# Kernel tuning notes

Measured on AMD Instinct MI355X. Metric: run time of the kernel, lower is better.

The kernel has to match this reference:

```python
import jax, jax.numpy as jnp
import numpy as np

B, DIM, HEADS, BLOCKS = 16, 192, 6, 6
H = W = 64
WS, SHIFT, MLP = 8, 4, 4
N = WS * WS
HD = DIM // HEADS
NW = (H // WS) * (W // WS)
SCALE = HD ** -0.5


def _ln(x, g, b, eps=1e-5):
    mu = jnp.mean(x, -1, keepdims=True)
    var = jnp.mean(jnp.square(x - mu), -1, keepdims=True)
    return (x - mu) * jax.lax.rsqrt(var + eps) * g + b


def _win_part(x):  # [B,H,W,C] -> [B*NW, N, C]
    x = x.reshape(B, H // WS, WS, W // WS, WS, DIM)
    return x.transpose(0, 1, 3, 2, 4, 5).reshape(-1, N, DIM)


def _win_rev(w):  # [B*NW, N, C] -> [B,H,W,C]
    x = w.reshape(B, H // WS, W // WS, WS, WS, DIM)
    return x.transpose(0, 1, 3, 2, 4, 5).reshape(B, H, W, DIM)


def _rel_pos_index():
    coords = np.stack(np.meshgrid(np.arange(WS), np.arange(WS), indexing='ij')).reshape(2, -1)
    rel = (coords[:, :, None] - coords[:, None, :]).transpose(1, 2, 0)
    rel[:, :, 0] += WS - 1
    rel[:, :, 1] += WS - 1
    rel[:, :, 0] *= 2 * WS - 1
    return jnp.asarray(rel.sum(-1))  # [N, N] int


def _attn_mask():  # shifted-window attention mask, [NW, N, N]
    img = np.zeros((H, W))
    cnt = 0
    for hs in (slice(0, -WS), slice(-WS, -SHIFT), slice(-SHIFT, None)):
        for ws_ in (slice(0, -WS), slice(-WS, -SHIFT), slice(-SHIFT, None)):
            img[hs, ws_] = cnt
            cnt += 1
    mw = img.reshape(H // WS, WS, W // WS, WS).transpose(0, 2, 1, 3).reshape(-1, N)
    am = mw[:, None, :] - mw[:, :, None]
    return jnp.asarray(np.where(am != 0, -100.0, 0.0).astype(np.float32))


RPI = _rel_pos_index()
MASK = _attn_mask()


def _block(x, shifted, n1g, n1b, qkvw, qkvb, pw, pb, rpb, n2g, n2b, f1w, f1b, f2w, f2b):
    shortcut = x  # [B, H*W, DIM]
    x = _ln(x, n1g, n1b).reshape(B, H, W, DIM)
    if shifted:
        x = jnp.roll(x, (-SHIFT, -SHIFT), (1, 2))
    xw = _win_part(x)  # [B*NW, N, DIM]
    qkv = (xw @ qkvw.T + qkvb).reshape(-1, N, 3, HEADS, HD).transpose(2, 0, 3, 1, 4)
    q, k, v = qkv[0], qkv[1], qkv[2]  # [B*NW, HEADS, N, HD]
    attn = jnp.einsum('bhnd,bhmd->bhnm', q * SCALE, k)
    attn = attn + rpb[RPI].transpose(2, 0, 1)[None]  # relative position bias
    if shifted:
        attn = (attn.reshape(B, NW, HEADS, N, N) + MASK[None, :, None]).reshape(-1, HEADS, N, N)
    attn = jax.nn.softmax(attn, -1)
    xw = jnp.einsum('bhnm,bhmd->bnhd', attn, v).reshape(-1, N, DIM)
    xw = xw @ pw.T + pb
    x = _win_rev(xw)
    if shifted:
        x = jnp.roll(x, (SHIFT, SHIFT), (1, 2))
    x = shortcut + x.reshape(B, H * W, DIM)
    h = _ln(x, n2g, n2b)
    h = jax.nn.gelu(h @ f1w.T + f1b, approximate=False) @ f2w.T + f2b
    return x + h


def _forward(x, en_g, en_b, n1_g, n1_b, qkv_w, qkv_b, proj_w, proj_b, rpb, n2_g, n2_b, fc1_w, fc1_b, fc2_w, fc2_b, fn_g, fn_b, conv_w):
    y = x.reshape(B, DIM, H * W).transpose(0, 2, 1)  # patch embed (patch_size=1)
    y = _ln(y, en_g, en_b)
    for i in range(BLOCKS):
        y = _block(y, i % 2 == 1, n1_g[i], n1_b[i], qkv_w[i], qkv_b[i], proj_w[i], proj_b[i],
                   rpb[i], n2_g[i], n2_b[i], fc1_w[i], fc1_b[i], fc2_w[i], fc2_b[i])
    y = _ln(y, fn_g, fn_b)
    y = y.transpose(0, 2, 1).reshape(B, DIM, H, W)  # patch unembed
    return y + jax.lax.conv_general_dilated(y, conv_w, (1, 1), 'SAME',
                                            dimension_numbers=('NCHW', 'OIHW', 'NCHW'))


def setup_inputs() -> dict:
    key = jax.random.key(0)
    ks = jax.random.split(key, 7)
    s = 0.02
    f32 = jnp.float32
    return {
        'x': jax.random.normal(ks[0], (B, DIM, H, W), f32),
        'en_g': jnp.ones((DIM,), f32), 'en_b': jnp.zeros((DIM,), f32),
        'n1_g': jnp.ones((BLOCKS, DIM), f32), 'n1_b': jnp.zeros((BLOCKS, DIM), f32),
        'qkv_w': s * jax.random.normal(ks[1], (BLOCKS, 3 * DIM, DIM), f32),
        'qkv_b': jnp.zeros((BLOCKS, 3 * DIM), f32),
        'proj_w': s * jax.random.normal(ks[2], (BLOCKS, DIM, DIM), f32),
        'proj_b': jnp.zeros((BLOCKS, DIM), f32),
        'rpb': s * jax.random.normal(ks[3], (BLOCKS, (2 * WS - 1) ** 2, HEADS), f32),
        'n2_g': jnp.ones((BLOCKS, DIM), f32), 'n2_b': jnp.zeros((BLOCKS, DIM), f32),
        'fc1_w': s * jax.random.normal(ks[4], (BLOCKS, MLP * DIM, DIM), f32),
        'fc1_b': jnp.zeros((BLOCKS, MLP * DIM), f32),
        'fc2_w': s * jax.random.normal(ks[5], (BLOCKS, DIM, MLP * DIM), f32),
        'fc2_b': jnp.zeros((BLOCKS, DIM), f32),
        'fn_g': jnp.ones((DIM,), f32), 'fn_b': jnp.zeros((DIM,), f32),
        'conv_w': s * jax.random.normal(ks[6], (DIM, DIM, 3, 3), f32),
    }


def reference(x, en_g, en_b, n1_g, n1_b, qkv_w, qkv_b, proj_w, proj_b, rpb, n2_g, n2_b, fc1_w, fc1_b, fc2_w, fc2_b, fn_g, fn_b, conv_w):
    return _forward(x, en_g, en_b, n1_g, n1_b, qkv_w, qkv_b, proj_w, proj_b, rpb,
                    n2_g, n2_b, fc1_w, fc1_b, fc2_w, fc2_b, fn_g, fn_b, conv_w)
```

## Files before the change

kernel.cpp:

```cpp
#include <hip/hip_runtime.h>
#include <cstdint>
#include <cstddef>

#define BATCH 16
#define DIM 192
#define HEADS 6
#define HD 32
#define TOK 65536
#define QKV_D 576
#define MLP_D 768
#define SCALE 0.17677669529663687f

#define CHQ 32768

typedef __bf16 bf16x8 __attribute__((ext_vector_type(8)));
typedef float f32x4 __attribute__((ext_vector_type(4)));

__device__ __forceinline__ unsigned short f2bf(float f) {
  union { float f; unsigned u; } c;
  c.f = f;
  return (unsigned short)((c.u + 0x7fffu + ((c.u >> 16) & 1)) >> 16);
}

__device__ __forceinline__ float waveSum(float v) {
#pragma unroll
  for (int off = 32; off; off >>= 1) v += __shfl_xor(v, off, 64);
  return v;
}

__device__ __forceinline__ float rowSum16(float v) {
  v += __shfl_xor(v, 1, 64);
  v += __shfl_xor(v, 2, 64);
  v += __shfl_xor(v, 4, 64);
  v += __shfl_xor(v, 8, 64);
  return v;
}

#define GLD(SRC, DST)                                                     \
  __builtin_amdgcn_global_load_lds(                                       \
      (const __attribute__((address_space(1))) void*)(SRC),               \
      (__attribute__((address_space(3))) void*)(DST), 16, 0, 0)

__global__ __launch_bounds__(64) void zero_k(float* p) { p[threadIdx.x] = 0.f; }

__global__ __launch_bounds__(256) void cvt_k(const float* __restrict__ s,
                                             unsigned short* __restrict__ d,
                                             int n) {
  int i = ((blockIdx.x << 8) + threadIdx.x) << 2;
  if (i < n) {
    float4 v = *(const float4*)(s + i);
    d[i] = f2bf(v.x);
    d[i + 1] = f2bf(v.y);
    d[i + 2] = f2bf(v.z);
    d[i + 3] = f2bf(v.w);
  }
}

__global__ __launch_bounds__(256) void cvt_qkv_k(const float* __restrict__ s,
                                                 unsigned short* __restrict__ d) {
  int i = (blockIdx.x << 8) + threadIdx.x;
  if (i < 663552) {
    int r = (i / 192) % 576;
    float v = s[i];
    if (r < 192) v *= SCALE;
    d[i] = f2bf(v);
  }
}

__global__ __launch_bounds__(256) void scale_qkvb_k(const float* __restrict__ s,
                                                    float* __restrict__ d) {
  int i = (blockIdx.x << 8) + threadIdx.x;
  if (i < 3456) {
    float v = s[i];
    if ((i % 576) < 192) v *= SCALE;
    d[i] = v;
  }
}

__global__ __launch_bounds__(256) void cvt_conv_k(const float* __restrict__ s,
                                                  unsigned short* __restrict__ d) {
  int i = (blockIdx.x << 8) + threadIdx.x;
  if (i < 331776) {
    int o = i / 1728;
    int r = i - o * 1728;
    int tap = r / 192;
    int ci = r - tap * 192;
    d[i] = f2bf(s[o * 1728 + ci * 9 + tap]);
  }
}

__global__ __launch_bounds__(256) void embed_ln_t_k(
    const float* __restrict__ x, const float* __restrict__ g,
    const float* __restrict__ be, float* __restrict__ y) {
  __shared__ float ts[192 * 65];
  const int w = threadIdx.x >> 6, lane = threadIdx.x & 63;
  const int t0 = blockIdx.x << 6;
  const int b = t0 >> 12, tb = t0 & 4095;
  const float* xb = x + (((size_t)b * DIM) << 12) + tb;
#pragma unroll
  for (int j = 0; j < 48; ++j) {
    int ch = w * 48 + j;
    ts[ch * 65 + lane] = xb[((size_t)ch << 12) + lane];
  }
  __syncthreads();
#pragma unroll 4
  for (int idx = 0; idx < 16; ++idx) {
    int tk = (w << 4) + idx;
    float v0 = ts[lane * 65 + tk];
    float v1 = ts[(lane + 64) * 65 + tk];
    float v2 = ts[(lane + 128) * 65 + tk];
    float mu = waveSum(v0 + v1 + v2) * (1.f / 192.f);
    float d0 = v0 - mu, d1 = v1 - mu, d2 = v2 - mu;
    float var = waveSum(d0 * d0 + d1 * d1 + d2 * d2) * (1.f / 192.f);
    float rs = rsqrtf(var + 1e-5f);
    float* yp = y + (size_t)(t0 + tk) * DIM;
    yp[lane] = d0 * rs * g[lane] + be[lane];
    yp[lane + 64] = d1 * rs * g[lane + 64] + be[lane + 64];
    yp[lane + 128] = d2 * rs * g[lane + 128] + be[lane + 128];
  }
}

__global__ __launch_bounds__(256) void ln_window_k(
    const float* __restrict__ y, const float* __restrict__ g,
    const float* __restrict__ be, unsigned short* __restrict__ xw,
    int shifted) {
  int m = (blockIdx.x << 2) + (threadIdx.x >> 6);
  int lane = threadIdx.x & 63;
  int widx = m >> 6, n = m & 63;
  int b = widx >> 6, win = widx & 63;
  int hp = ((win >> 3) << 3) + (n >> 3);
  int wp = ((win & 7) << 3) + (n & 7);
  if (shifted) { hp = (hp + 4) & 63; wp = (wp + 4) & 63; }
  int src = (b << 12) + (hp << 6) + wp;
  const float* yp = y + (size_t)src * DIM;
  float v0 = yp[lane], v1 = yp[lane + 64], v2 = yp[lane + 128];
  float mu = waveSum(v0 + v1 + v2) * (1.f / 192.f);
  float d0 = v0 - mu, d1 = v1 - mu, d2 = v2 - mu;
  float var = waveSum(d0 * d0 + d1 * d1 + d2 * d2) * (1.f / 192.f);
  float rs = rsqrtf(var + 1e-5f);
  unsigned short* op = xw + (size_t)m * DIM;
  op[lane] = f2bf(d0 * rs * g[lane] + be[lane]);
  op[lane + 64] = f2bf(d1 * rs * g[lane + 64] + be[lane + 64]);
  op[lane + 128] = f2bf(d2 * rs * g[lane + 128] + be[lane + 128]);
}

__global__ __launch_bounds__(64) void attn_k(
    const unsigned short* __restrict__ qkv, const float* __restrict__ rpb,
    unsigned short* __restrict__ out, int shifted, int widx0) {
  __shared__ unsigned short vt[32 * 72];
  __shared__ unsigned short pl[64 * 72];
  __shared__ float rp[228];
  const int lwidx = blockIdx.x / HEADS;
  const int head = blockIdx.x - lwidx * HEADS;
  const int l = threadIdx.x;
  const int g = l >> 4, li = l & 15;

  for (int i = l; i < 225; i += 64) rp[i] = rpb[i * HEADS + head];

  const unsigned short* base = qkv + (size_t)lwidx * 64 * QKV_D + head * HD;

  bf16x8 qf[4], kf[4];
#pragma unroll
  for (int n = 0; n < 4; ++n)
    qf[n] = *(const bf16x8*)(base + (size_t)(16 * n + li) * QKV_D + g * 8);
#pragma unroll
  for (int i = 0; i < 4; ++i)
    kf[i] = *(const bf16x8*)(base + (size_t)(16 * i + li) * QKV_D + DIM + g * 8);

#pragma unroll
  for (int p = 0; p < 4; ++p) {
    int r = 16 * p + (l >> 2);
    int d0 = (l & 3) << 3;
    bf16x8 v8 = *(const bf16x8*)(base + (size_t)r * QKV_D + 2 * DIM + d0);
#pragma unroll
    for (int e = 0; e < 8; ++e)
      vt[(d0 + e) * 72 + r] = ((const unsigned short*)&v8)[e];
  }

  f32x4 s[4][4] = {};
#pragma unroll
  for (int i = 0; i < 4; ++i)
#pragma unroll
    for (int n = 0; n < 4; ++n)
      s[i][n] = __builtin_amdgcn_mfma_f32_16x16x32_bf16(kf[i], qf[n], s[i][n],
                                                        0, 0, 0);
  __syncthreads();

  const int win = (widx0 + lwidx) & 63;
  const int wh = (win >> 3) << 3, wwp = (win & 7) << 3;
  int rq[4], cq[4], zq[4];
#pragma unroll
  for (int n = 0; n < 4; ++n) {
    int q = 16 * n + li;
    rq[n] = q >> 3;
    cq[n] = q & 7;
    zq[n] = 0;
    if (shifted) {
      int hq = wh + rq[n], wq = wwp + cq[n];
      int zr = hq < 56 ? 0 : (hq < 60 ? 1 : 2);
      int zc = wq < 56 ? 0 : (wq < 60 ? 1 : 2);
      zq[n] = 3 * zr + zc;
    }
  }
#pragma unroll
  for (int i = 0; i < 4; ++i)
#pragma unroll
    for (int j = 0; j < 4; ++j) {
      int m = 16 * i + 4 * g + j;
      int rm = m >> 3, cm = m & 7;
      int zm = 0;
      if (shifted) {
        int hm = wh + rm, wm = wwp + cm;
        int zr = hm < 56 ? 0 : (hm < 60 ? 1 : 2);
        int zc = wm < 56 ? 0 : (wm < 60 ? 1 : 2);
        zm = 3 * zr + zc;
      }
#pragma unroll
      for (int n = 0; n < 4; ++n) {
        float b = rp[(rq[n] - rm + 7) * 15 + (cq[n] - cm + 7)];
        if (shifted && zm != zq[n]) b -= 100.f;
        s[i][n][j] += b;
      }
    }

  float inv[4];
#pragma unroll
  for (int n = 0; n < 4; ++n) {
    float m0 = -1e30f;
#pragma unroll
    for (int i = 0; i < 4; ++i)
#pragma unroll
      for (int j = 0; j < 4; ++j) m0 = fmaxf(m0, s[i][n][j]);
    m0 = fmaxf(m0, __shfl_xor(m0, 16, 64));
    m0 = fmaxf(m0, __shfl_xor(m0, 32, 64));
    float s0 = 0.f;
#pragma unroll
    for (int i = 0; i < 4; ++i)
#pragma unroll
      for (int j = 0; j < 4; ++j) {
        float e = __expf(s[i][n][j] - m0);
        s[i][n][j] = e;
        s0 += e;
      }
    s0 += __shfl_xor(s0, 16, 64);
    s0 += __shfl_xor(s0, 32, 64);
    inv[n] = 1.f / s0;
  }

#pragma unroll
  for (int n = 0; n < 4; ++n) {
    int q = 16 * n + li;
#pragma unroll
    for (int i = 0; i < 4; ++i) {
      unsigned lo = (unsigned)f2bf(s[i][n][0]) | ((unsigned)f2bf(s[i][n][1]) << 16);
      unsigned hi = (unsigned)f2bf(s[i][n][2]) | ((unsigned)f2bf(s[i][n][3]) << 16);
      *(uint2*)&pl[q * 72 + 16 * i + 4 * g] = uint2{lo, hi};
    }
  }
  __syncthreads();

  f32x4 o[2][4] = {};
#pragma unroll
  for (int ks = 0; ks < 2; ++ks) {
    bf16x8 va[2], pb[4];
#pragma unroll
    for (int i2 = 0; i2 < 2; ++i2)
      va[i2] = *(const bf16x8*)&vt[(16 * i2 + li) * 72 + 32 * ks + 8 * g];
#pragma unroll
    for (int n2 = 0; n2 < 4; ++n2)
      pb[n2] = *(const bf16x8*)&pl[(16 * n2 + li) * 72 + 32 * ks + 8 * g];
#pragma unroll
    for (int i2 = 0; i2 < 2; ++i2)
#pragma unroll
      for (int n2 = 0; n2 < 4; ++n2)
        o[i2][n2] = __builtin_amdgcn_mfma_f32_16x16x32_bf16(va[i2], pb[n2],
                                                            o[i2][n2], 0, 0, 0);
  }

  unsigned short* ob = out + (size_t)(lwidx * 64) * DIM + head * HD;
#pragma unroll
  for (int i2 = 0; i2 < 2; ++i2)
#pragma unroll
    for (int n2 = 0; n2 < 4; ++n2) {
      int q = 16 * n2 + li;
      float iv = inv[n2];
      unsigned lo = (unsigned)f2bf(o[i2][n2][0] * iv) |
                    ((unsigned)f2bf(o[i2][n2][1] * iv) << 16);
      unsigned hi = (unsigned)f2bf(o[i2][n2][2] * iv) |
                    ((unsigned)f2bf(o[i2][n2][3] * iv) << 16);
      *(uint2*)(ob + (size_t)q * DIM + 16 * i2 + 4 * g) = uint2{lo, hi};
    }
}

__device__ __forceinline__ void mfma_block256(const unsigned short* As,
                                              const unsigned short* Bs,
                                              f32x4 acc[4][4], int w,
                                              int lane) {
  const int frow = lane & 15;
  const int fk = (lane >> 4) << 3;
#pragma unroll
  for (int kk = 0; kk < 64; kk += 32) {
    int slotk = (kk + fk) >> 3;
    bf16x8 a[4], b[4];
#pragma unroll
    for (int m = 0; m < 4; ++m) {
      int ar = (w << 6) + (m << 4) + frow;
      a[m] = *(const bf16x8*)&As[(ar << 6) + ((slotk ^ (ar & 7)) << 3)];
    }
#pragma unroll
    for (int n = 0; n < 4; ++n) {
      int br = (n << 4) + frow;
      b[n] = *(const bf16x8*)&Bs[(br << 6) + ((slotk ^ (br & 7)) << 3)];
    }
#pragma unroll
    for (int m = 0; m < 4; ++m)
#pragma unroll
      for (int n = 0; n < 4; ++n)
        acc[m][n] =
            __builtin_amdgcn_mfma_f32_16x16x32_bf16(a[m], b[n], acc[m][n], 0,
                                                    0, 0);
  }
}

__device__ __forceinline__ void mfma_block128(const unsigned short* As,
                                              const unsigned short* Bs,
                                              f32x4 acc[2][4], int w,
                                              int lane) {
  const int frow = lane & 15;
  const int fk = (lane >> 4) << 3;
#pragma unroll
  for (int kk = 0; kk < 64; kk += 32) {
    int slotk = (kk + fk) >> 3;
    int ar0 = (w << 5) + frow, ar1 = ar0 + 16;
    bf16x8 a0 = *(const bf16x8*)&As[(ar0 << 6) + ((slotk ^ (ar0 & 7)) << 3)];
    bf16x8 a1 = *(const bf16x8*)&As[(ar1 << 6) + ((slotk ^ (ar1 & 7)) << 3)];
    bf16x8 b[4];
#pragma unroll
    for (int n = 0; n < 4; ++n) {
      int br = (n << 4) + frow;
      b[n] = *(const bf16x8*)&Bs[(br << 6) + ((slotk ^ (br & 7)) << 3)];
    }
#pragma unroll
    for (int n = 0; n < 4; ++n) {
      acc[0][n] = __builtin_amdgcn_mfma_f32_16x16x32_bf16(a0, b[n], acc[0][n], 0, 0, 0);
      acc[1][n] = __builtin_amdgcn_mfma_f32_16x16x32_bf16(a1, b[n], acc[1][n], 0, 0, 0);
    }
  }
}

template <int EPI>
__global__ __launch_bounds__(256) void mgemm_k(
    const unsigned short* __restrict__ A, const unsigned short* __restrict__ W,
    const float* __restrict__ bias, void* __restrict__ Cv, int N, int K) {
  __shared__ unsigned short As[256 * 64];
  __shared__ unsigned short Bs[64 * 64];
  const int tid = threadIdx.x;
  const int w = tid >> 6, lane = tid & 63;
  const int row0 = blockIdx.x << 8;
  const int col0 = blockIdx.y << 6;
  f32x4 acc[4][4] = {};

  for (int k0 = 0; k0 < K; k0 += 64) {
    if (k0) __syncthreads();
#pragma unroll
    for (int r = 0; r < 2; ++r) {
      int q = (r << 8) + tid;
      int brow = q >> 3, cs = q & 7;
      int kg = cs ^ (brow & 7);
      GLD(W + (size_t)(col0 + brow) * K + k0 + (kg << 3),
          Bs + (((r << 8) + (w << 6)) << 3));
    }
#pragma unroll
    for (int r = 0; r < 8; ++r) {
      int q = (r << 8) + tid;
      int arow = q >> 3, cs = q & 7;
      int kg = cs ^ (arow & 7);
      GLD(A + (size_t)(row0 + arow) * K + k0 + (kg << 3),
          As + (((r << 8) + (w << 6)) << 3));
    }
    __syncthreads();
    mfma_block256(As, Bs, acc, w, lane);
  }

  const int erow = (lane >> 4) << 2;
  const int ecol = lane & 15;
#pragma unroll
  for (int mr = 0; mr < 4; ++mr)
#pragma unroll
    for (int nr = 0; nr < 4; ++nr)
#pragma unroll
      for (int j = 0; j < 4; ++j) {
        int row = row0 + (w << 6) + (mr << 4) + erow + j;
        int col = col0 + (nr << 4) + ecol;
        float v = acc[mr][nr][j];
        ((unsigned short*)Cv)[(size_t)row * N + col] = f2bf(v + bias[col]);
      }
}

template <int LAST>
__global__ __launch_bounds__(256) void pm_k(
    const unsigned short* __restrict__ A, const unsigned short* __restrict__ Wp,
    const float* __restrict__ bp, const float* __restrict__ g2,
    const float* __restrict__ be2, const unsigned short* __restrict__ W1,
    const float* __restrict__ b1, const unsigned short* __restrict__ W2,
    const float* __restrict__ b2, float* __restrict__ y,
    unsigned short* __restrict__ lnout, const float* __restrict__ g1,
    const float* __restrict__ be1, int sh_cur, int sh_next) {
  __shared__ unsigned short a2[64 * 192];
  __shared__ unsigned short Wb1[64 * 192];
  __shared__ unsigned short Wb2[192 * 64];
  __shared__ unsigned short hc[64 * 64];
  const int tid = threadIdx.x;
  const int w = tid >> 6, lane = tid & 63;
  const int row0 = blockIdx.x << 6;
  const int frow = lane & 15;
  const int fk = (lane >> 4) << 3;
  const int erow = (lane >> 4) << 2;
  const int ecol = lane & 15;

  bf16x8 ap[6];
  {
    const unsigned short* arp = A + (size_t)(row0 + (w << 4) + frow) * 192 + fk;
#pragma unroll
    for (int t = 0; t < 6; ++t) ap[t] = *(const bf16x8*)(arp + t * 32);
  }

  f32x4 accp[12] = {};
#pragma unroll
  for (int k0 = 0; k0 < 192; k0 += 64) {
    __syncthreads();
#pragma unroll
    for (int r = 0; r < 6; ++r) {
      int q = (r << 8) + tid;
      int rw = q >> 3, cs = q & 7;
      int kg = cs ^ (rw & 7);
      GLD(Wp + (size_t)rw * 192 + k0 + (kg << 3),
          Wb2 + (((r << 8) + (w << 6)) << 3));
    }
    __syncthreads();
#pragma unroll
    for (int kk2 = 0; kk2 < 64; kk2 += 32) {
      int slotk = (kk2 + fk) >> 3;
      int t = (k0 + kk2) >> 5;
#pragma unroll
      for (int n = 0; n < 12; ++n) {
        int br = (n << 4) + frow;
        bf16x8 b = *(const bf16x8*)&Wb2[(br << 6) + ((slotk ^ (br & 7)) << 3)];
        accp[n] =
            __builtin_amdgcn_mfma_f32_16x16x32_bf16(ap[t], b, accp[n], 0, 0, 0);
      }
    }
  }

  int tokj[4];
  {
    float bpv[12], gv2[12], bv2[12];
#pragma unroll
    for (int n = 0; n < 12; ++n) {
      int col = (n << 4) + ecol;
      bpv[n] = bp[col];
      gv2[n] = g2[col];
      bv2[n] = be2[col];
    }
#pragma unroll
    for (int j = 0; j < 4; ++j) {
      int m = row0 + (w << 4) + erow + j;
      int n64 = m & 63, widx = m >> 6;
      int bl = widx >> 6, win = widx & 63;
      int hp = ((win >> 3) << 3) + (n64 >> 3);
      int wp2 = ((win & 7) << 3) + (n64 & 7);
      if (sh_cur) { hp = (hp + 4) & 63; wp2 = (wp2 + 4) & 63; }
      int tok = (bl << 12) + (hp << 6) + wp2;
      tokj[j] = tok;
      const float* yp = y + (size_t)tok * DIM;
      float s0 = 0.f;
#pragma unroll
      for (int n = 0; n < 12; ++n) {
        float v = accp[n][j] + bpv[n] + yp[(n << 4) + ecol];
        accp[n][j] = v;
        s0 += v;
      }
      float mu = rowSum16(s0) * (1.f / 192.f);
      float s1 = 0.f;
#pragma unroll
      for (int n = 0; n < 12; ++n) {
        float d = accp[n][j] - mu;
        s1 += d * d;
      }
      float rs = rsqrtf(rowSum16(s1) * (1.f / 192.f) + 1e-5f);
      int hr = (w << 4) + erow + j;
#pragma unroll
      for (int n = 0; n < 12; ++n) {
        int col = (n << 4) + ecol;
        unsigned short lv = f2bf((accp[n][j] - mu) * rs * gv2[n] + bv2[n]);
        int kb = col >> 6, c64 = col & 63;
        a2[(kb << 12) + (hr << 6) + (((c64 >> 3) ^ (hr & 7)) << 3) + (c64 & 7)] =
            lv;
      }
    }
  }
  {
    int ar = (w << 4) + frow;
#pragma unroll
    for (int t = 0; t < 6; ++t) {
      int kb = t >> 1;
      int slotk = (((t & 1) << 5) + fk) >> 3;
      ap[t] = *(const bf16x8*)&a2[(kb << 12) + (ar << 6) +
                                  ((slotk ^ (ar & 7)) << 3)];
    }
  }

  f32x4 acc2[12] = {};
  for (int n0 = 0; n0 < 12; ++n0) {
    __syncthreads();
#pragma unroll
    for (int r = 0; r < 6; ++r) {
      int q = (r << 8) + tid;
      int kb = q >> 9, rw = (q >> 3) & 63, cs = q & 7;
      int kg = cs ^ (rw & 7);
      GLD(W1 + (size_t)(n0 * 64 + rw) * 192 + kb * 64 + (kg << 3),
          Wb1 + (((r << 8) + (w << 6)) << 3));
    }
#pragma unroll
    for (int r = 0; r < 6; ++r) {
      int q = (r << 8) + tid;
      int rw = q >> 3, cs = q & 7;
      int kg = cs ^ (rw & 7);
      GLD(W2 + (size_t)rw * 768 + n0 * 64 + (kg << 3),
          Wb2 + (((r << 8) + (w << 6)) << 3));
    }
    __syncthreads();
    f32x4 acc1[4] = {};
#pragma unroll
    for (int kk = 0; kk < 192; kk += 32) {
      int kb = kk >> 6;
      int slotk = ((kk & 63) + fk) >> 3;
#pragma unroll
      for (int n = 0; n < 4; ++n) {
        int br = (n << 4) + frow;
        bf16x8 b = *(const bf16x8*)&Wb1[(kb << 12) + (br << 6) +
                                        ((slotk ^ (br & 7)) << 3)];
        acc1[n] = __builtin_amdgcn_mfma_f32_16x16x32_bf16(ap[kk >> 5], b,
                                                          acc1[n], 0, 0, 0);
      }
    }
#pragma unroll
    for (int n = 0; n < 4; ++n) {
      float bb = b1[n0 * 64 + (n << 4) + ecol];
#pragma unroll
      for (int j = 0; j < 4; ++j) {
        int hr = (w << 4) + erow + j;
        int hcol = (n << 4) + ecol;
        float xg = acc1[n][j] + bb;
        float x3 = xg * xg * xg;
        float t1 = fmaf(0.044715f, x3, xg);
        float e = __expf(t1 * -1.5957691216057308f);
        float hv = xg * __builtin_amdgcn_rcpf(1.f + e);
        hc[(hr << 6) + (((hcol >> 3) ^ (hr & 7)) << 3) + (hcol & 7)] = f2bf(hv);
      }
    }
#pragma unroll
    for (int kk = 0; kk < 64; kk += 32) {
      int slotk = (kk + fk) >> 3;
      int ar = (w << 4) + frow;
      bf16x8 a = *(const bf16x8*)&hc[(ar << 6) + ((slotk ^ (ar & 7)) << 3)];
#pragma unroll
      for (int n = 0; n < 12; ++n) {
        int br = (n << 4) + frow;
        bf16x8 b = *(const bf16x8*)&Wb2[(br << 6) + ((slotk ^ (br & 7)) << 3)];
        acc2[n] =
            __builtin_amdgcn_mfma_f32_16x16x32_bf16(a, b, acc2[n], 0, 0, 0);
      }
    }
  }

  float b2v[12], gv[12], bev[12];
#pragma unroll
  for (int n = 0; n < 12; ++n) {
    int col = (n << 4) + ecol;
    b2v[n] = b2[col];
    gv[n] = g1[col];
    bev[n] = be1[col];
  }
#pragma unroll
  for (int j = 0; j < 4; ++j) {
    int tok = tokj[j];
    float* yp = y + (size_t)tok * DIM;
    float v[12];
    float s0 = 0.f;
#pragma unroll
    for (int n = 0; n < 12; ++n) {
      v[n] = accp[n][j] + acc2[n][j] + b2v[n];
      s0 += v[n];
    }
    float mu = rowSum16(s0) * (1.f / 192.f);
    float s1 = 0.f;
#pragma unroll
    for (int n = 0; n < 12; ++n) {
      float d = v[n] - mu;
      s1 += d * d;
    }
    float rs = rsqrtf(rowSum16(s1) * (1.f / 192.f) + 1e-5f);
    if (LAST == 0) {
#pragma unroll
      for (int n = 0; n < 12; ++n) yp[(n << 4) + ecol] = v[n];
      int hw = tok & 4095, gi = tok >> 12;
      int h = hw >> 6, ww2 = hw & 63;
      int hs = sh_next ? (h + 60) & 63 : h;
      int ws = sh_next ? (ww2 + 60) & 63 : ww2;
      int win = ((hs >> 3) << 3) | (ws >> 3);
      int n64 = ((hs & 7) << 3) | (ws & 7);
      size_t drow = ((size_t)gi << 12) + (win << 6) + n64;
      unsigned short* op = lnout + drow * DIM;
#pragma unroll
      for (int n = 0; n < 12; ++n)
        op[(n << 4) + ecol] = f2bf((v[n] - mu) * rs * gv[n] + bev[n]);
    } else {
      unsigned short* op = lnout + (size_t)tok * DIM;
#pragma unroll
      for (int n = 0; n < 12; ++n) {
        float r = (v[n] - mu) * rs * gv[n] + bev[n];
        yp[(n << 4) + ecol] = r;
        op[(n << 4) + ecol] = f2bf(r);
      }
    }
  }
}

__global__ __launch_bounds__(256) void conv_k(
    const unsigned short* __restrict__ A, const unsigned short* __restrict__ W,
    float* __restrict__ out, const float* __restrict__ Z,
    const unsigned short* __restrict__ zpg) {
  __shared__ unsigned short As[128 * 64];
  __shared__ unsigned short Bs[64 * 64];
  const int tid = threadIdx.x;
  const int w = tid >> 6, lane = tid & 63;
  const int row0 = blockIdx.x << 7;
  const int col0 = blockIdx.y << 6;
  f32x4 acc[2][4] = {};
  bool first = true;

#pragma unroll
  for (int tap = 0; tap < 9; ++tap) {
    const int dh = tap / 3 - 1, dw = tap % 3 - 1;
#pragma unroll
    for (int k0 = 0; k0 < 192; k0 += 64) {
      if (!first) __syncthreads();
      first = false;
#pragma unroll
      for (int r = 0; r < 2; ++r) {
        int q = (r << 8) + tid;
        int brow = q >> 3, cs = q & 7;
        int kg = cs ^ (brow & 7);
        GLD(W + (size_t)(col0 + brow) * 1728 + tap * 192 + k0 + (kg << 3),
            Bs + (((r << 8) + (w << 6)) << 3));
      }
#pragma unroll
      for (int r = 0; r < 4; ++r) {
        int q = (r << 8) + tid;
        int arow = q >> 3, cs = q & 7;
        int kg = cs ^ (arow & 7);
        int m = row0 + arow;
        int hw_ = m & 4095;
        int h = hw_ >> 6, ww = hw_ & 63;
        int ih = h + dh, iw = ww + dw;
        const unsigned short* src =
            ((unsigned)ih < 64u && (unsigned)iw < 64u)
                ? A + (size_t)(m + dh * 64 + dw) * DIM + k0 + (kg << 3)
                : zpg;
        GLD(src, As + (((r << 8) + (w << 6)) << 3));
      }
      __syncthreads();
      mfma_block128(As, Bs, acc, w, lane);
    }
  }

  const int erow = (lane >> 4) << 2;
  const int ecol = lane & 15;
#pragma unroll
  for (int mr = 0; mr < 2; ++mr)
#pragma unroll
    for (int nr = 0; nr < 4; ++nr)
#pragma unroll
      for (int j = 0; j < 4; ++j) {
        int row = row0 + (w << 5) + (mr << 4) + erow + j;
        int col = col0 + (nr << 4) + ecol;
        int b = row >> 12, hw_ = row & 4095;
        out[(((size_t)(b * DIM + col)) << 12) + hw_] =
            acc[mr][nr][j] + Z[(size_t)row * DIM + col];
      }
}

extern "C" void kernel_launch(void* const* d_in, const int* in_sizes, int n_in,
                              void* d_out, int out_size, void* d_ws,
                              size_t ws_size, hipStream_t stream) {
  const float* x = (const float*)d_in[0];
  const float* en_g = (const float*)d_in[1];
  const float* en_b = (const float*)d_in[2];
  const float* n1_g = (const float*)d_in[3];
  const float* n1_b = (const float*)d_in[4];
  const float* qkv_w = (const float*)d_in[5];
  const float* qkv_b = (const float*)d_in[6];
  const float* proj_w = (const float*)d_in[7];
  const float* proj_b = (const float*)d_in[8];
  const float* rpb = (const float*)d_in[9];
  const float* n2_g = (const float*)d_in[10];
  const float* n2_b = (const float*)d_in[11];
  const float* fc1_w = (const float*)d_in[12];
  const float* fc1_b = (const float*)d_in[13];
  const float* fc2_w = (const float*)d_in[14];
  const float* fc2_b = (const float*)d_in[15];
  const float* fn_g = (const float*)d_in[16];
  const float* fn_b = (const float*)d_in[17];
  const float* conv_w = (const float*)d_in[18];
  float* out = (float*)d_out;

  float* y = (float*)d_ws;
  unsigned short* buf1a = (unsigned short*)((char*)d_ws + 50331648);
  unsigned short* buf1b = (unsigned short*)((char*)d_ws + 75497472);
  unsigned short* wbuf = (unsigned short*)((char*)d_ws + 100663296);
  unsigned short* zpg = (unsigned short*)((char*)d_ws + 106635264);
  float* qkv_bs = (float*)((char*)d_ws + 106635520);
  unsigned short* qkvbuf = (unsigned short*)d_out;

  unsigned short* qkv_wb = wbuf;
  unsigned short* proj_wb = wbuf + 663552;
  unsigned short* fc1_wb = wbuf + 884736;
  unsigned short* fc2_wb = wbuf + 1769472;
  unsigned short* conv_wb = wbuf + 2654208;

  zero_k<<<1, 64, 0, stream>>>((float*)zpg);
  cvt_qkv_k<<<2592, 256, 0, stream>>>(qkv_w, qkv_wb);
  scale_qkvb_k<<<14, 256, 0, stream>>>(qkv_b, qkv_bs);
  cvt_k<<<216, 256, 0, stream>>>(proj_w, proj_wb, 221184);
  cvt_k<<<864, 256, 0, stream>>>(fc1_w, fc1_wb, 884736);
  cvt_k<<<864, 256, 0, stream>>>(fc2_w, fc2_wb, 884736);
  cvt_conv_k<<<1296, 256, 0, stream>>>(conv_w, conv_wb);

  embed_ln_t_k<<<1024, 256, 0, stream>>>(x, en_g, en_b, y);
  ln_window_k<<<16384, 256, 0, stream>>>(y, n1_g, n1_b, buf1a, 0);

  for (int i = 0; i < 6; ++i) {
    int sh = i & 1;
    unsigned short* bufA = (i & 1) ? buf1b : buf1a;
    unsigned short* bufB = (i & 1) ? buf1a : buf1b;
    for (int c = 0; c < 2; ++c) {
      unsigned short* bAc = bufA + (size_t)c * CHQ * DIM;
      mgemm_k<3><<<dim3(CHQ / 256, 9), 256, 0, stream>>>(
          bAc, qkv_wb + (size_t)i * QKV_D * DIM, qkv_bs + i * QKV_D, qkvbuf,
          QKV_D, DIM);
      attn_k<<<(CHQ / 64) * HEADS, 64, 0, stream>>>(
          qkvbuf, rpb + i * 225 * HEADS, bAc, sh, c * (CHQ / 64));
    }
    if (i < 5) {
      pm_k<0><<<TOK / 64, 256, 0, stream>>>(
          bufA, proj_wb + (size_t)i * DIM * DIM, proj_b + i * DIM,
          n2_g + i * DIM, n2_b + i * DIM, fc1_wb + (size_t)i * MLP_D * DIM,
          fc1_b + i * MLP_D, fc2_wb + (size_t)i * DIM * MLP_D, fc2_b + i * DIM,
          y, bufB, n1_g + (i + 1) * DIM, n1_b + (i + 1) * DIM, sh, (i + 1) & 1);
    } else {
      pm_k<1><<<TOK / 64, 256, 0, stream>>>(
          bufA, proj_wb + (size_t)i * DIM * DIM, proj_b + i * DIM,
          n2_g + i * DIM, n2_b + i * DIM, fc1_wb + (size_t)i * MLP_D * DIM,
          fc1_b + i * MLP_D, fc2_wb + (size_t)i * DIM * MLP_D, fc2_b + i * DIM,
          y, bufB, fn_g, fn_b, sh, 0);
    }
  }

  conv_k<<<dim3(TOK / 128, 3), 256, 0, stream>>>(buf1a, conv_wb, out, y, zpg);
}
```

Baseline: 1.167 ms.

## Shrink pm_k shared memory by aliasing weight buffers and staging LN output through hc

The fused proj+LN+MLP kernel previously used four LDS arrays of roughly 80 KB in total. It now keeps one 24 KB weight buffer shared by the proj, fc1 and fc2 weight tiles, and routes the LN2 output through the small hc buffer one 64-column chunk at a time. The aim is to cut LDS per block so more blocks can be resident per CU and latency is better hidden. In exchange, the W2 load is serialized after fc1 and GELU with two extra barriers per iteration, so it no longer overlaps the W1 load. The hc staging loop as written also has no barrier between chunk reuses, which may race across waves.

After: 1.622 ms. 1.39x slower.

```diff
diff --git a/kernel.cpp b/kernel.cpp
--- a/kernel.cpp
+++ b/kernel.cpp
@@ -406,9 +406,7 @@
     const float* __restrict__ b2, float* __restrict__ y,
     unsigned short* __restrict__ lnout, const float* __restrict__ g1,
     const float* __restrict__ be1, int sh_cur, int sh_next) {
-  __shared__ unsigned short a2[64 * 192];
-  __shared__ unsigned short Wb1[64 * 192];
-  __shared__ unsigned short Wb2[192 * 64];
+  __shared__ unsigned short Wsh[192 * 64];
   __shared__ unsigned short hc[64 * 64];
   const int tid = threadIdx.x;
   const int w = tid >> 6, lane = tid & 63;
@@ -435,7 +433,7 @@
       int rw = q >> 3, cs = q & 7;
       int kg = cs ^ (rw & 7);
       GLD(Wp + (size_t)rw * 192 + k0 + (kg << 3),
-          Wb2 + (((r << 8) + (w << 6)) << 3));
+          Wsh + (((r << 8) + (w << 6)) << 3));
     }
     __syncthreads();
 #pragma unroll
@@ -445,7 +443,7 @@
 #pragma unroll
       for (int n = 0; n < 12; ++n) {
         int br = (n << 4) + frow;
-        bf16x8 b = *(const bf16x8*)&Wb2[(br << 6) + ((slotk ^ (br & 7)) << 3)];
+        bf16x8 b = *(const bf16x8*)&Wsh[(br << 6) + ((slotk ^ (br & 7)) << 3)];
         accp[n] =
             __builtin_amdgcn_mfma_f32_16x16x32_bf16(ap[t], b, accp[n], 0, 0, 0);
       }
@@ -453,8 +451,10 @@
   }
 
   int tokj[4];
+  float muj[4], rsj[4];
+  float gv2[12], bv2[12];
   {
-    float bpv[12], gv2[12], bv2[12];
+    float bpv[12];
 #pragma unroll
     for (int n = 0; n < 12; ++n) {
       int col = (n << 4) + ecol;
@@ -487,26 +487,30 @@
         float d = accp[n][j] - mu;
         s1 += d * d;
       }
-      float rs = rsqrtf(rowSum16(s1) * (1.f / 192.f) + 1e-5f);
-      int hr = (w << 4) + erow + j;
-#pragma unroll
-      for (int n = 0; n < 12; ++n) {
-        int col = (n << 4) + ecol;
-        unsigned short lv = f2bf((accp[n][j] - mu) * rs * gv2[n] + bv2[n]);
-        int kb = col >> 6, c64 = col & 63;
-        a2[(kb << 12) + (hr << 6) + (((c64 >> 3) ^ (hr & 7)) << 3) + (c64 & 7)] =
-            lv;
-      }
-    }
-  }
-  {
+      muj[j] = mu;
+      rsj[j] = rsqrtf(rowSum16(s1) * (1.f / 192.f) + 1e-5f);
+    }
+  }
+#pragma unroll
+  for (int kb = 0; kb < 3; ++kb) {
+#pragma unroll
+    for (int n2 = 0; n2 < 4; ++n2) {
+      int n = kb * 4 + n2;
+#pragma unroll
+      for (int j = 0; j < 4; ++j) {
+        int hr = (w << 4) + erow + j;
+        int c64 = (n2 << 4) + ecol;
+        unsigned short lv =
+            f2bf((accp[n][j] - muj[j]) * rsj[j] * gv2[n] + bv2[n]);
+        hc[(hr << 6) + (((c64 >> 3) ^ (hr & 7)) << 3) + (c64 & 7)] = lv;
+      }
+    }
     int ar = (w << 4) + frow;
 #pragma unroll
-    for (int t = 0; t < 6; ++t) {
-      int kb = t >> 1;
-      int slotk = (((t & 1) << 5) + fk) >> 3;
-      ap[t] = *(const bf16x8*)&a2[(kb << 12) + (ar << 6) +
-                                  ((slotk ^ (ar & 7)) << 3)];
+    for (int t2 = 0; t2 < 2; ++t2) {
+      int slotk = ((t2 << 5) + fk) >> 3;
+      ap[kb * 2 + t2] =
+          *(const bf16x8*)&hc[(ar << 6) + ((slotk ^ (ar & 7)) << 3)];
     }
   }
 
@@ -519,15 +523,7 @@
       int kb = q >> 9, rw = (q >> 3) & 63, cs = q & 7;
       int kg = cs ^ (rw & 7);
       GLD(W1 + (size_t)(n0 * 64 + rw) * 192 + kb * 64 + (kg << 3),
-          Wb1 + (((r << 8) + (w << 6)) << 3));
-    }
-#pragma unroll
-    for (int r = 0; r < 6; ++r) {
-      int q = (r << 8) + tid;
-      int rw = q >> 3, cs = q & 7;
-      int kg = cs ^ (rw & 7);
-      GLD(W2 + (size_t)rw * 768 + n0 * 64 + (kg << 3),
-          Wb2 + (((r << 8) + (w << 6)) << 3));
+          Wsh + (((r << 8) + (w << 6)) << 3));
     }
     __syncthreads();
     f32x4 acc1[4] = {};
@@ -538,7 +534,7 @@
 #pragma unroll
       for (int n = 0; n < 4; ++n) {
         int br = (n << 4) + frow;
-        bf16x8 b = *(const bf16x8*)&Wb1[(kb << 12) + (br << 6) +
+        bf16x8 b = *(const bf16x8*)&Wsh[(kb << 12) + (br << 6) +
                                         ((slotk ^ (br & 7)) << 3)];
         acc1[n] = __builtin_amdgcn_mfma_f32_16x16x32_bf16(ap[kk >> 5], b,
                                                           acc1[n], 0, 0, 0);
@@ -559,6 +555,16 @@
         hc[(hr << 6) + (((hcol >> 3) ^ (hr & 7)) << 3) + (hcol & 7)] = f2bf(hv);
       }
     }
+    __syncthreads();
+#pragma unroll
+    for (int r = 0; r < 6; ++r) {
+      int q = (r << 8) + tid;
+      int rw = q >> 3, cs = q & 7;
+      int kg = cs ^ (rw & 7);
+      GLD(W2 + (size_t)rw * 768 + n0 * 64 + (kg << 3),
+          Wsh + (((r << 8) + (w << 6)) << 3));
+    }
+    __syncthreads();
 #pragma unroll
     for (int kk = 0; kk < 64; kk += 32) {
       int slotk = (kk + fk) >> 3;
@@ -567,7 +573,7 @@
 #pragma unroll
       for (int n = 0; n < 12; ++n) {
         int br = (n << 4) + frow;
-        bf16x8 b = *(const bf16x8*)&Wb2[(br << 6) + ((slotk ^ (br & 7)) << 3)];
+        bf16x8 b = *(const bf16x8*)&Wsh[(br << 6) + ((slotk ^ (br & 7)) << 3)];
         acc2[n] =
             __builtin_amdgcn_mfma_f32_16x16x32_bf16(a, b, acc2[n], 0, 0, 0);
       }
```
